# Performance work log

Measured on AMD Instinct MI355X. Metric: run time of the kernel, lower is better.

Reference implementation:

```python
import jax, jax.numpy as jnp
import numpy as np

THRESHOLD = 0.9
HALF_PI = float(np.pi / 2.0)


def _flatten_chw(x):
    # [1, C, H, W] -> [H*W, C] (matches squeeze().reshape((C,-1)).T)
    c = x.shape[1]
    return x.reshape(c, -1).T


def _make_grid(h, w, dtype):
    # (row, col) index per flattened cell, row-major to match reshape order
    ii, jj = jnp.meshgrid(jnp.arange(h, dtype=dtype), jnp.arange(w, dtype=dtype), indexing='ij')
    return jnp.stack([ii.reshape(-1), jj.reshape(-1)], axis=-1)  # [H*W, 2]


def _decode_head(bboxes, class_scores, objectness, orient, anchor_dims):
    h, w = bboxes.shape[2], bboxes.shape[3]
    bb = _flatten_chw(bboxes)            # [N, 7]
    cs = _flatten_chw(class_scores)      # [N, num_classes]
    obj = _flatten_chw(objectness)       # [N, 1]
    grid = _make_grid(h, w, bb.dtype) + 0.5  # [N, 2]

    # NMS-lite: objectness thresholding expressed as a mask (jit-safe, no
    # data-dependent shapes; suppressed rows are zeroed instead of dropped).
    mask = (obj[:, 0] >= THRESHOLD).astype(bb.dtype)  # [N]

    # bbox decode: orient + sigmoid(xy)+grid, sigmoid(z), anchor_dims*exp(dims)
    orient_col = orient + jax.nn.sigmoid(bb[:, 0:1]) * HALF_PI  # [N, 1]
    xyz = jax.nn.sigmoid(bb[:, 1:4])                             # [N, 3]
    xy = xyz[:, 0:2] + grid
    z = xyz[:, 2:3]
    dims = anchor_dims[None, :] * jnp.exp(bb[:, 4:7])            # [N, 3]
    boxes = jnp.concatenate([orient_col, xy, z, dims], axis=-1)  # [N, 7]

    m = mask[:, None]
    return boxes * m, cs * m, obj * m, mask


def setup_inputs() -> dict:
    key = jax.random.key(0)
    ks = jax.random.split(key, 7)
    H = W = 1024
    C = 8
    return {
        'pred_objectness1': jax.random.uniform(ks[0], (1, 1, H, W), dtype=jnp.float32),
        'pred_class_scores1': jax.random.normal(ks[1], (1, C, H, W), dtype=jnp.float32),
        'pred_bboxes1': jax.random.normal(ks[2], (1, 7, H, W), dtype=jnp.float32),
        'pred_objectness2': jax.random.uniform(ks[3], (1, 1, H, W), dtype=jnp.float32),
        'pred_class_scores2': jax.random.normal(ks[4], (1, C, H, W), dtype=jnp.float32),
        'pred_bboxes2': jax.random.normal(ks[5], (1, 7, H, W), dtype=jnp.float32),
        'anchor_orients': jax.random.uniform(ks[6], (2,), dtype=jnp.float32) * HALF_PI,
        'anchor_dims': jnp.asarray([1.6, 3.9, 1.56], dtype=jnp.float32),
    }


def reference(pred_objectness1, pred_class_scores1, pred_bboxes1,
              pred_objectness2, pred_class_scores2, pred_bboxes2,
              anchor_orients, anchor_dims):
    boxes1, scores1, obj1, mask1 = _decode_head(
        pred_bboxes1, pred_class_scores1, pred_objectness1, anchor_orients[0], anchor_dims)
    boxes2, scores2, obj2, mask2 = _decode_head(
        pred_bboxes2, pred_class_scores2, pred_objectness2, anchor_orients[1], anchor_dims)
    return (boxes1, scores1, obj1, mask1, boxes2, scores2, obj2, mask2)
```

## Files before the change

### kernel.cpp

```cpp
#include <hip/hip_runtime.h>

#define NLOC (1024 * 1024)
#define HALF_PI 1.57079632679489662f
#define THRESH 0.9f

__device__ __forceinline__ float sigmoidf_(float x) {
    return 1.0f / (1.0f + __expf(-x));
}

__global__ __launch_bounds__(256) void decode_kernel(
    const float* __restrict__ obj1, const float* __restrict__ cs1, const float* __restrict__ bb1,
    const float* __restrict__ obj2, const float* __restrict__ cs2, const float* __restrict__ bb2,
    const float* __restrict__ orients, const float* __restrict__ adims,
    float* __restrict__ out)
{
    __shared__ float lds[4 * 2048];

    const int tid  = threadIdx.x;
    const int wid  = tid >> 6;
    const int lane = tid & 63;
    const int head = blockIdx.x >> 10;
    const int blk  = blockIdx.x & 1023;
    const int wl   = (blk << 10) + (wid << 8);
    const int n0   = wl + (lane << 2);

    float* buf = &lds[wid << 11];

    const float* obj = head ? obj2 : obj1;
    const float* cs  = head ? cs2  : cs1;
    const float* bb  = head ? bb2  : bb1;
    const float orient = orients[head];
    const float d0 = adims[0], d1 = adims[1], d2 = adims[2];
    float* ob = out + (size_t)head * 17 * NLOC;

    float4 o4 = *reinterpret_cast<const float4*>(obj + n0);
    float ov[4] = { o4.x, o4.y, o4.z, o4.w };

    float bbv[7][4];
#pragma unroll
    for (int c = 0; c < 7; ++c) {
        float4 t = *reinterpret_cast<const float4*>(bb + (size_t)c * NLOC + n0);
        bbv[c][0] = t.x; bbv[c][1] = t.y; bbv[c][2] = t.z; bbv[c][3] = t.w;
    }
    float sv[8][4];
#pragma unroll
    for (int c = 0; c < 8; ++c) {
        float4 t = *reinterpret_cast<const float4*>(cs + (size_t)c * NLOC + n0);
        sv[c][0] = t.x; sv[c][1] = t.y; sv[c][2] = t.z; sv[c][3] = t.w;
    }

    const float fi  = (float)(n0 >> 10) + 0.5f;
    const float fj0 = (float)(n0 & 1023) + 0.5f;

    float mk_[4];
    float bx[28];
#pragma unroll
    for (int t = 0; t < 4; ++t) {
        float m  = (ov[t] >= THRESH) ? 1.0f : 0.0f;
        mk_[t] = m;
        float fj = fj0 + (float)t;
        bx[t * 7 + 0] = (orient + sigmoidf_(bbv[0][t]) * HALF_PI) * m;
        bx[t * 7 + 1] = (sigmoidf_(bbv[1][t]) + fi) * m;
        bx[t * 7 + 2] = (sigmoidf_(bbv[2][t]) + fj) * m;
        bx[t * 7 + 3] = sigmoidf_(bbv[3][t]) * m;
        bx[t * 7 + 4] = d0 * __expf(bbv[4][t]) * m;
        bx[t * 7 + 5] = d1 * __expf(bbv[5][t]) * m;
        bx[t * 7 + 6] = d2 * __expf(bbv[6][t]) * m;
    }

    *reinterpret_cast<float4*>(ob + (size_t)15 * NLOC + n0) =
        make_float4(ov[0] * mk_[0], ov[1] * mk_[1], ov[2] * mk_[2], ov[3] * mk_[3]);
    *reinterpret_cast<float4*>(ob + (size_t)16 * NLOC + n0) =
        make_float4(mk_[0], mk_[1], mk_[2], mk_[3]);

#pragma unroll
    for (int q = 0; q < 7; ++q)
        *reinterpret_cast<float4*>(&buf[lane * 28 + q * 4]) =
            make_float4(bx[q * 4 + 0], bx[q * 4 + 1], bx[q * 4 + 2], bx[q * 4 + 3]);
    {
        float* gb = ob + (size_t)wl * 7;
#pragma unroll
        for (int q = 0; q < 7; ++q) {
            int w = 4 * (lane + 64 * q);
            *reinterpret_cast<float4*>(gb + w) = *reinterpret_cast<const float4*>(&buf[w]);
        }
    }

#pragma unroll
    for (int q = 0; q < 8; ++q) {
        int t = q >> 1, c0 = (q & 1) * 4;
        float m = mk_[t];
        int f = lane * 8 + q;
        int p = f ^ ((f >> 3) & 7);
        *reinterpret_cast<float4*>(&buf[p * 4]) =
            make_float4(sv[c0][t] * m, sv[c0 + 1][t] * m, sv[c0 + 2][t] * m, sv[c0 + 3][t] * m);
    }
    {
        float* gs = ob + (size_t)7 * NLOC + (size_t)wl * 8;
#pragma unroll
        for (int q = 0; q < 8; ++q) {
            int f = lane + 64 * q;
            int p = f ^ ((f >> 3) & 7);
            *reinterpret_cast<float4*>(gs + 4 * f) =
                *reinterpret_cast<const float4*>(&buf[p * 4]);
        }
    }
}

extern "C" void kernel_launch(void* const* d_in, const int* in_sizes, int n_in,
                              void* d_out, int out_size, void* d_ws, size_t ws_size,
                              hipStream_t stream) {
    const float* obj1    = (const float*)d_in[0];
    const float* cs1     = (const float*)d_in[1];
    const float* bb1     = (const float*)d_in[2];
    const float* obj2    = (const float*)d_in[3];
    const float* cs2     = (const float*)d_in[4];
    const float* bb2     = (const float*)d_in[5];
    const float* orients = (const float*)d_in[6];
    const float* adims   = (const float*)d_in[7];
    float* out = (float*)d_out;

    decode_kernel<<<2048, 256, 0, stream>>>(obj1, cs1, bb1, obj2, cs2, bb2,
                                            orients, adims, out);
}
```

Measured before the change: 52.48 us.

## Process both heads per block with software prefetch and nontemporal stores

Each block now decodes both heads for its tile, issuing the second head's loads before the first head's LDS-transposed stores so memory latency overlaps. Output writes use nontemporal stores to avoid cache pollution, and explicit wave-level fences order the LDS reuse. The grid is halved and launch bounds request more occupancy, but the extra prefetched registers may limit occupancy and fewer blocks reduce parallelism.

Measured after the change: 45.79 us. 1.15x faster.

```diff
diff --git a/kernel.cpp b/kernel.cpp
--- a/kernel.cpp
+++ b/kernel.cpp
@@ -4,11 +4,28 @@
 #define HALF_PI 1.57079632679489662f
 #define THRESH 0.9f
 
+typedef float v4f __attribute__((ext_vector_type(4)));
+
 __device__ __forceinline__ float sigmoidf_(float x) {
     return 1.0f / (1.0f + __expf(-x));
 }
 
-__global__ __launch_bounds__(256) void decode_kernel(
+__device__ __forceinline__ void nt_store4(float* p, float a, float b, float c, float d) {
+    v4f v = { a, b, c, d };
+    __builtin_nontemporal_store(v, reinterpret_cast<v4f*>(p));
+}
+
+__device__ __forceinline__ void nt_copy4(float* g, const float* l) {
+    v4f v = *reinterpret_cast<const v4f*>(l);
+    __builtin_nontemporal_store(v, reinterpret_cast<v4f*>(g));
+}
+
+__device__ __forceinline__ void wave_lds_fence() {
+    __builtin_amdgcn_fence(__ATOMIC_ACQ_REL, "wavefront");
+    __builtin_amdgcn_wave_barrier();
+}
+
+__global__ __launch_bounds__(256, 4) void decode_kernel(
     const float* __restrict__ obj1, const float* __restrict__ cs1, const float* __restrict__ bb1,
     const float* __restrict__ obj2, const float* __restrict__ cs2, const float* __restrict__ bb2,
     const float* __restrict__ orients, const float* __restrict__ adims,
@@ -19,90 +36,152 @@
     const int tid  = threadIdx.x;
     const int wid  = tid >> 6;
     const int lane = tid & 63;
-    const int head = blockIdx.x >> 10;
-    const int blk  = blockIdx.x & 1023;
-    const int wl   = (blk << 10) + (wid << 8);
+    const int wl   = ((int)blockIdx.x << 10) + (wid << 8);
     const int n0   = wl + (lane << 2);
-
     float* buf = &lds[wid << 11];
 
-    const float* obj = head ? obj2 : obj1;
-    const float* cs  = head ? cs2  : cs1;
-    const float* bb  = head ? bb2  : bb1;
-    const float orient = orients[head];
     const float d0 = adims[0], d1 = adims[1], d2 = adims[2];
-    float* ob = out + (size_t)head * 17 * NLOC;
-
-    float4 o4 = *reinterpret_cast<const float4*>(obj + n0);
-    float ov[4] = { o4.x, o4.y, o4.z, o4.w };
-
-    float bbv[7][4];
-#pragma unroll
-    for (int c = 0; c < 7; ++c) {
-        float4 t = *reinterpret_cast<const float4*>(bb + (size_t)c * NLOC + n0);
-        bbv[c][0] = t.x; bbv[c][1] = t.y; bbv[c][2] = t.z; bbv[c][3] = t.w;
-    }
-    float sv[8][4];
-#pragma unroll
-    for (int c = 0; c < 8; ++c) {
-        float4 t = *reinterpret_cast<const float4*>(cs + (size_t)c * NLOC + n0);
-        sv[c][0] = t.x; sv[c][1] = t.y; sv[c][2] = t.z; sv[c][3] = t.w;
-    }
+    const float or0 = orients[0], or1 = orients[1];
+    float* ob0 = out;
+    float* ob1 = out + (size_t)17 * NLOC;
 
     const float fi  = (float)(n0 >> 10) + 0.5f;
     const float fj0 = (float)(n0 & 1023) + 0.5f;
 
-    float mk_[4];
+    float4 o0 = *reinterpret_cast<const float4*>(obj1 + n0);
+    float4 b0[7];
+#pragma unroll
+    for (int c = 0; c < 7; ++c)
+        b0[c] = *reinterpret_cast<const float4*>(bb1 + (size_t)c * NLOC + n0);
+    float4 s0[8];
+#pragma unroll
+    for (int c = 0; c < 8; ++c)
+        s0[c] = *reinterpret_cast<const float4*>(cs1 + (size_t)c * NLOC + n0);
+
+    float ov0[4] = { o0.x, o0.y, o0.z, o0.w };
+    float mk0[4];
     float bx[28];
 #pragma unroll
     for (int t = 0; t < 4; ++t) {
-        float m  = (ov[t] >= THRESH) ? 1.0f : 0.0f;
-        mk_[t] = m;
+        float m = (ov0[t] >= THRESH) ? 1.0f : 0.0f;
+        mk0[t] = m;
         float fj = fj0 + (float)t;
-        bx[t * 7 + 0] = (orient + sigmoidf_(bbv[0][t]) * HALF_PI) * m;
-        bx[t * 7 + 1] = (sigmoidf_(bbv[1][t]) + fi) * m;
-        bx[t * 7 + 2] = (sigmoidf_(bbv[2][t]) + fj) * m;
-        bx[t * 7 + 3] = sigmoidf_(bbv[3][t]) * m;
-        bx[t * 7 + 4] = d0 * __expf(bbv[4][t]) * m;
-        bx[t * 7 + 5] = d1 * __expf(bbv[5][t]) * m;
-        bx[t * 7 + 6] = d2 * __expf(bbv[6][t]) * m;
-    }
-
-    *reinterpret_cast<float4*>(ob + (size_t)15 * NLOC + n0) =
-        make_float4(ov[0] * mk_[0], ov[1] * mk_[1], ov[2] * mk_[2], ov[3] * mk_[3]);
-    *reinterpret_cast<float4*>(ob + (size_t)16 * NLOC + n0) =
-        make_float4(mk_[0], mk_[1], mk_[2], mk_[3]);
+        bx[t * 7 + 0] = (or0 + sigmoidf_(((const float*)&b0[0])[t]) * HALF_PI) * m;
+        bx[t * 7 + 1] = (sigmoidf_(((const float*)&b0[1])[t]) + fi) * m;
+        bx[t * 7 + 2] = (sigmoidf_(((const float*)&b0[2])[t]) + fj) * m;
+        bx[t * 7 + 3] = sigmoidf_(((const float*)&b0[3])[t]) * m;
+        bx[t * 7 + 4] = d0 * __expf(((const float*)&b0[4])[t]) * m;
+        bx[t * 7 + 5] = d1 * __expf(((const float*)&b0[5])[t]) * m;
+        bx[t * 7 + 6] = d2 * __expf(((const float*)&b0[6])[t]) * m;
+    }
+    nt_store4(ob0 + (size_t)15 * NLOC + n0,
+              ov0[0] * mk0[0], ov0[1] * mk0[1], ov0[2] * mk0[2], ov0[3] * mk0[3]);
+    nt_store4(ob0 + (size_t)16 * NLOC + n0, mk0[0], mk0[1], mk0[2], mk0[3]);
 
 #pragma unroll
     for (int q = 0; q < 7; ++q)
         *reinterpret_cast<float4*>(&buf[lane * 28 + q * 4]) =
             make_float4(bx[q * 4 + 0], bx[q * 4 + 1], bx[q * 4 + 2], bx[q * 4 + 3]);
-    {
-        float* gb = ob + (size_t)wl * 7;
+
+    float4 o1 = *reinterpret_cast<const float4*>(obj2 + n0);
+    float4 b1[7];
+#pragma unroll
+    for (int c = 0; c < 7; ++c)
+        b1[c] = *reinterpret_cast<const float4*>(bb2 + (size_t)c * NLOC + n0);
+
+    wave_lds_fence();
+    {
+        float* gb = ob0 + (size_t)wl * 7;
 #pragma unroll
         for (int q = 0; q < 7; ++q) {
             int w = 4 * (lane + 64 * q);
-            *reinterpret_cast<float4*>(gb + w) = *reinterpret_cast<const float4*>(&buf[w]);
-        }
-    }
+            nt_copy4(gb + w, &buf[w]);
+        }
+    }
+    wave_lds_fence();
 
 #pragma unroll
     for (int q = 0; q < 8; ++q) {
         int t = q >> 1, c0 = (q & 1) * 4;
-        float m = mk_[t];
+        float m = mk0[t];
         int f = lane * 8 + q;
         int p = f ^ ((f >> 3) & 7);
         *reinterpret_cast<float4*>(&buf[p * 4]) =
-            make_float4(sv[c0][t] * m, sv[c0 + 1][t] * m, sv[c0 + 2][t] * m, sv[c0 + 3][t] * m);
-    }
-    {
-        float* gs = ob + (size_t)7 * NLOC + (size_t)wl * 8;
+            make_float4(((const float*)&s0[c0 + 0])[t] * m, ((const float*)&s0[c0 + 1])[t] * m,
+                        ((const float*)&s0[c0 + 2])[t] * m, ((const float*)&s0[c0 + 3])[t] * m);
+    }
+
+    float4 s1[8];
+#pragma unroll
+    for (int c = 0; c < 8; ++c)
+        s1[c] = *reinterpret_cast<const float4*>(cs2 + (size_t)c * NLOC + n0);
+
+    wave_lds_fence();
+    {
+        float* gs = ob0 + (size_t)7 * NLOC + (size_t)wl * 8;
 #pragma unroll
         for (int q = 0; q < 8; ++q) {
             int f = lane + 64 * q;
             int p = f ^ ((f >> 3) & 7);
-            *reinterpret_cast<float4*>(gs + 4 * f) =
-                *reinterpret_cast<const float4*>(&buf[p * 4]);
+            nt_copy4(gs + 4 * f, &buf[p * 4]);
+        }
+    }
+    wave_lds_fence();
+
+    float ov1[4] = { o1.x, o1.y, o1.z, o1.w };
+    float mk1[4];
+#pragma unroll
+    for (int t = 0; t < 4; ++t) {
+        float m = (ov1[t] >= THRESH) ? 1.0f : 0.0f;
+        mk1[t] = m;
+        float fj = fj0 + (float)t;
+        bx[t * 7 + 0] = (or1 + sigmoidf_(((const float*)&b1[0])[t]) * HALF_PI) * m;
+        bx[t * 7 + 1] = (sigmoidf_(((const float*)&b1[1])[t]) + fi) * m;
+        bx[t * 7 + 2] = (sigmoidf_(((const float*)&b1[2])[t]) + fj) * m;
+        bx[t * 7 + 3] = sigmoidf_(((const float*)&b1[3])[t]) * m;
+        bx[t * 7 + 4] = d0 * __expf(((const float*)&b1[4])[t]) * m;
+        bx[t * 7 + 5] = d1 * __expf(((const float*)&b1[5])[t]) * m;
+        bx[t * 7 + 6] = d2 * __expf(((const float*)&b1[6])[t]) * m;
+    }
+    nt_store4(ob1 + (size_t)15 * NLOC + n0,
+              ov1[0] * mk1[0], ov1[1] * mk1[1], ov1[2] * mk1[2], ov1[3] * mk1[3]);
+    nt_store4(ob1 + (size_t)16 * NLOC + n0, mk1[0], mk1[1], mk1[2], mk1[3]);
+
+#pragma unroll
+    for (int q = 0; q < 7; ++q)
+        *reinterpret_cast<float4*>(&buf[lane * 28 + q * 4]) =
+            make_float4(bx[q * 4 + 0], bx[q * 4 + 1], bx[q * 4 + 2], bx[q * 4 + 3]);
+
+    wave_lds_fence();
+    {
+        float* gb = ob1 + (size_t)wl * 7;
+#pragma unroll
+        for (int q = 0; q < 7; ++q) {
+            int w = 4 * (lane + 64 * q);
+            nt_copy4(gb + w, &buf[w]);
+        }
+    }
+    wave_lds_fence();
+
+#pragma unroll
+    for (int q = 0; q < 8; ++q) {
+        int t = q >> 1, c0 = (q & 1) * 4;
+        float m = mk1[t];
+        int f = lane * 8 + q;
+        int p = f ^ ((f >> 3) & 7);
+        *reinterpret_cast<float4*>(&buf[p * 4]) =
+            make_float4(((const float*)&s1[c0 + 0])[t] * m, ((const float*)&s1[c0 + 1])[t] * m,
+                        ((const float*)&s1[c0 + 2])[t] * m, ((const float*)&s1[c0 + 3])[t] * m);
+    }
+
+    wave_lds_fence();
+    {
+        float* gs = ob1 + (size_t)7 * NLOC + (size_t)wl * 8;
+#pragma unroll
+        for (int q = 0; q < 8; ++q) {
+            int f = lane + 64 * q;
+            int p = f ^ ((f >> 3) & 7);
+            nt_copy4(gs + 4 * f, &buf[p * 4]);
         }
     }
 }
@@ -120,6 +199,6 @@
     const float* adims   = (const float*)d_in[7];
     float* out = (float*)d_out;
 
-    decode_kernel<<<2048, 256, 0, stream>>>(obj1, cs1, bb1, obj2, cs2, bb2,
+    decode_kernel<<<1024, 256, 0, stream>>>(obj1, cs1, bb1, obj2, cs2, bb2,
                                             orients, adims, out);
 }
```
